# Performance work log

Measured on AMD Instinct MI355X. Metric: run time of the kernel, lower is better.

Reference implementation:

```python
import jax, jax.numpy as jnp
import numpy as np

B, S, D, H = 2, 2048, 1024, 16
HD = D // H  # 64
SOFT_CAP = 50.0
MAX_WAVELENGTH = 10000.0


def apply_rope(x, positions, head_dim):
    # x: [B,S,H,hd], positions: [B,S]
    fraction = 2.0 * jnp.arange(head_dim // 2, dtype=jnp.float32) / head_dim
    timescale = MAX_WAVELENGTH ** fraction                      # [hd/2]
    sinusoid = positions.astype(jnp.float32)[..., None] / timescale  # [B,S,hd/2]
    sin = jnp.sin(sinusoid)[..., None, :]                       # [B,S,1,hd/2]
    cos = jnp.cos(sinusoid)[..., None, :]
    first, second = jnp.split(x, 2, axis=-1)
    out = jnp.concatenate(
        [first * cos - second * sin, second * cos + first * sin], axis=-1)
    return out.astype(x.dtype)


def setup_inputs() -> dict:
    key = jax.random.key(0)
    k1, k2, k3 = jax.random.split(key, 3)
    inputs = jax.random.normal(k1, (B, S, D), jnp.float32)
    segment_positions = jnp.tile(jnp.arange(S, dtype=jnp.int32), (B, 1))
    mask = jnp.tril(jnp.ones((S, S), dtype=bool))[None, None]   # causal [1,1,S,S]
    w_in = jax.random.normal(k2, (D, H, 3 * HD), jnp.float32) * 0.02
    w_out = jax.random.normal(k3, (H, HD, D), jnp.float32) * 0.02
    return {"inputs": inputs, "segment_positions": segment_positions,
            "mask": mask, "w_in": w_in, "w_out": w_out}


def reference(inputs, segment_positions, mask, w_in, w_out):
    # fused QKV projection: [B,S,H,3*hd]
    proj = jnp.einsum('bsd,dhe->bshe', inputs, w_in)
    q, k, v = jnp.split(proj, 3, axis=-1)
    q = apply_rope(q, segment_positions, HD)
    k = apply_rope(k, segment_positions, HD)
    q = q / jnp.sqrt(jnp.float32(HD))
    attn = jnp.einsum('bqhd,bkhd->bhqk', q, k)                  # [B,H,S,S]
    big_neg = jnp.finfo(jnp.float32).min
    attn = jnp.where(mask, attn, big_neg)
    attn = jnp.tanh(attn / SOFT_CAP) * SOFT_CAP                 # soft-cap AFTER mask
    attn = jax.nn.softmax(attn, axis=-1)
    x = jnp.einsum('bhqk,bkhd->bqhd', attn, v)
    return jnp.einsum('bqhd,hdo->bqo', x, w_out)
```

## Files before the change

kernel.cpp:

```cpp
#include <hip/hip_runtime.h>
#include <math.h>

#define BB 2
#define SS 2048
#define DD 1024
#define HH 16
#define HDIM 64
#define BS (BB*SS)
#define NQKV (HH*3*HDIM)
#define PERHEAD ((size_t)SS*HDIM)

typedef __attribute__((ext_vector_type(8))) short bf16x8;
typedef __attribute__((ext_vector_type(4))) float f32x4;

typedef const __attribute__((address_space(1))) unsigned int ga_u32;
typedef __attribute__((address_space(3))) unsigned int lds_u32;

__device__ inline short f2bf(float x) {
    union { float f; unsigned u; } v; v.f = x;
    unsigned r = v.u + 0x7FFF + ((v.u >> 16) & 1);
    return (short)(r >> 16);
}

__device__ inline void gl_lds16(const void* g, void* l) {
    __builtin_amdgcn_global_load_lds((ga_u32*)g, (lds_u32*)l, 16, 0, 0);
}

__global__ __launch_bounds__(256)
void convert_bf16(const float* __restrict__ A, unsigned short* __restrict__ Ab)
{
    int i = (blockIdx.x * 256 + threadIdx.x) * 4;
    float4 v = *(const float4*)&A[i];
    ushort4 o;
    o.x = (unsigned short)f2bf(v.x); o.y = (unsigned short)f2bf(v.y);
    o.z = (unsigned short)f2bf(v.z); o.w = (unsigned short)f2bf(v.w);
    *(ushort4*)&Ab[i] = o;
}

__global__ __launch_bounds__(256)
void transpose_bf16(const float* __restrict__ W, unsigned short* __restrict__ Wt,
                    int K, int N)
{
    __shared__ float tile[64][65];
    const int k0 = blockIdx.y * 64, n0 = blockIdx.x * 64;
    const int t = threadIdx.x;
    #pragma unroll
    for (int i = 0; i < 4; ++i) {
        int lin = t + 256 * i;
        int r = lin >> 4, c4 = (lin & 15) << 2;
        float4 v = *(const float4*)&W[(size_t)(k0 + r) * N + n0 + c4];
        tile[r][c4] = v.x; tile[r][c4 + 1] = v.y;
        tile[r][c4 + 2] = v.z; tile[r][c4 + 3] = v.w;
    }
    __syncthreads();
    #pragma unroll
    for (int i = 0; i < 4; ++i) {
        int lin = t + 256 * i;
        int n = lin >> 4, c4 = (lin & 15) << 2;
        ushort4 o;
        o.x = (unsigned short)f2bf(tile[c4 + 0][n]);
        o.y = (unsigned short)f2bf(tile[c4 + 1][n]);
        o.z = (unsigned short)f2bf(tile[c4 + 2][n]);
        o.w = (unsigned short)f2bf(tile[c4 + 3][n]);
        *(ushort4*)&Wt[(size_t)(n0 + n) * K + k0 + c4] = o;
    }
}

template<int QKV>
__global__ __launch_bounds__(256)
void gemm_mfma(const unsigned short* __restrict__ A,
               const unsigned short* __restrict__ Bt,
               float* __restrict__ C,
               float* __restrict__ Qp, float* __restrict__ Kp,
               unsigned short* __restrict__ Vb,
               int M, int N, int K)
{
    __shared__ __align__(16) unsigned short As[128 * 32];
    __shared__ __align__(16) unsigned short Bs[128 * 32];
    const int t = threadIdx.x;
    const int wave = t >> 6, lane = t & 63;
    const int quad = lane >> 4, lc = lane & 15;
    const int bm = blockIdx.y * 128, bn = blockIdx.x * 128;
    const int wr = wave >> 1, wc = wave & 1;

    const int srow0 = wave * 32 + (lane >> 2);
    const int srow1 = srow0 + 16;
    const int sc = (lane & 3) ^ ((lane >> 3) & 3);
    const unsigned short* aptr0 = A  + (size_t)(bm + srow0) * K + sc * 8;
    const unsigned short* aptr1 = A  + (size_t)(bm + srow1) * K + sc * 8;
    const unsigned short* bptr0 = Bt + (size_t)(bn + srow0) * K + sc * 8;
    const unsigned short* bptr1 = Bt + (size_t)(bn + srow1) * K + sc * 8;
    unsigned short* alds0 = &As[(wave * 32)      * 32];
    unsigned short* alds1 = &As[(wave * 32 + 16) * 32];
    unsigned short* blds0 = &Bs[(wave * 32)      * 32];
    unsigned short* blds1 = &Bs[(wave * 32 + 16) * 32];

    const int cx = quad ^ ((lc >> 1) & 3);

    f32x4 acc[4][4] = {};

    for (int k0 = 0; k0 < K; k0 += 32) {
        gl_lds16(aptr0 + k0, alds0);
        gl_lds16(aptr1 + k0, alds1);
        gl_lds16(bptr0 + k0, blds0);
        gl_lds16(bptr1 + k0, blds1);
        __syncthreads();

        bf16x8 af[4], bfr[4];
        #pragma unroll
        for (int rt = 0; rt < 4; ++rt)
            af[rt] = *(const bf16x8*)&As[(wr * 64 + rt * 16 + lc) * 32 + cx * 8];
        #pragma unroll
        for (int nt = 0; nt < 4; ++nt)
            bfr[nt] = *(const bf16x8*)&Bs[(wc * 64 + nt * 16 + lc) * 32 + cx * 8];
        #pragma unroll
        for (int rt = 0; rt < 4; ++rt)
            #pragma unroll
            for (int nt = 0; nt < 4; ++nt)
                acc[rt][nt] = __builtin_amdgcn_mfma_f32_16x16x32_bf16(
                    af[rt], bfr[nt], acc[rt][nt], 0, 0, 0);
        __syncthreads();
    }

    if (QKV) {
        #pragma unroll
        for (int rt = 0; rt < 4; ++rt) {
            #pragma unroll
            for (int reg = 0; reg < 4; ++reg) {
                int m = bm + wr * 64 + rt * 16 + quad * 4 + reg;
                int b = m >> 11, s = m & 2047;
                #pragma unroll
                for (int nt = 0; nt < 4; ++nt) {
                    int n = bn + wc * 64 + nt * 16 + lc;
                    int h = n / 192, r = n % 192;
                    float v = acc[rt][nt][reg];
                    if (r < 64) {
                        Qp[(((size_t)(b * HH + h)) * SS + s) * HDIM + r] = v;
                    } else if (r < 128) {
                        Kp[(((size_t)(b * HH + h)) * SS + s) * HDIM + r - 64] = v;
                    } else {
                        Vb[(((size_t)(b * HH + h)) * HDIM + (r - 128)) * SS + s] =
                            (unsigned short)f2bf(v);
                    }
                }
            }
        }
    } else {
        #pragma unroll
        for (int rt = 0; rt < 4; ++rt)
            #pragma unroll
            for (int reg = 0; reg < 4; ++reg) {
                int m = bm + wr * 64 + rt * 16 + quad * 4 + reg;
                #pragma unroll
                for (int nt = 0; nt < 4; ++nt) {
                    int n = bn + wc * 64 + nt * 16 + lc;
                    C[(size_t)m * N + n] = acc[rt][nt][reg];
                }
            }
    }
}

__global__ __launch_bounds__(256)
void rope_kernel(const float* __restrict__ Qf, const float* __restrict__ Kf,
                 unsigned short* __restrict__ Qb, unsigned short* __restrict__ Kb,
                 const int* __restrict__ pos)
{
    int tid = blockIdx.x * 256 + threadIdx.x;
    int i = tid & 31;
    int s = (tid >> 5) & 2047;
    int h = (tid >> 16) & 15;
    int b = tid >> 20;
    float p  = (float)pos[b * SS + s];
    float ts = powf(10000.0f, (float)i / 32.0f);
    float ang = p / ts;
    float sn, cs;
    sincosf(ang, &sn, &cs);
    size_t base = (((size_t)(b * HH + h)) * SS + s) * HDIM;
    float q1 = Qf[base + i], q2 = Qf[base + 32 + i];
    Qb[base + i]      = (unsigned short)f2bf((q1 * cs - q2 * sn) * 0.125f);
    Qb[base + 32 + i] = (unsigned short)f2bf((q2 * cs + q1 * sn) * 0.125f);
    float k1 = Kf[base + i], k2 = Kf[base + 32 + i];
    Kb[base + i]      = (unsigned short)f2bf(k1 * cs - k2 * sn);
    Kb[base + 32 + i] = (unsigned short)f2bf(k2 * cs + k1 * sn);
}

__global__ __launch_bounds__(256)
void attn_mfma_kernel(const unsigned short* __restrict__ Qb,
                      const unsigned short* __restrict__ Kb,
                      const unsigned short* __restrict__ Vb,
                      unsigned short* __restrict__ Xb)
{
    __shared__ __align__(16) unsigned short Ks[64 * 64];
    __shared__ __align__(16) unsigned short Vs[64 * 64];
    __shared__ __align__(16) unsigned short Ps[4][16][72];

    const int t    = threadIdx.x;
    const int wave = t >> 6, lane = t & 63;
    const int quad = lane >> 4, lc = lane & 15;
    const int bid  = blockIdx.x;
    const int qt   = 31 - (bid >> 5);
    const int bh   = bid & 31;
    const int b    = bh >> 4, h = bh & 15;

    const unsigned short* Qbase = Qb + ((size_t)bh * SS + (size_t)(qt * 64 + wave * 16)) * HDIM;
    const unsigned short* Kbase = Kb + (size_t)bh * PERHEAD;
    const unsigned short* Vbase = Vb + (size_t)bh * PERHEAD;

    bf16x8 qf[2];
    qf[0] = *(const bf16x8*)&Qbase[lc * HDIM + quad * 8];
    qf[1] = *(const bf16x8*)&Qbase[lc * HDIM + 32 + quad * 8];

    const int r8 = lane >> 3, c8 = lane & 7, gcs = c8 ^ r8;
    const unsigned short* ksrc0 = Kbase + (size_t)(wave * 16 + r8) * HDIM + gcs * 8;
    const unsigned short* ksrc1 = ksrc0 + 8 * HDIM;
    unsigned short* kdst0 = &Ks[(wave * 16) * 64];
    unsigned short* kdst1 = &Ks[(wave * 16 + 8) * 64];
    const unsigned short* vsrc0 = Vbase + (size_t)(wave * 16 + r8) * SS + gcs * 8;
    const unsigned short* vsrc1 = vsrc0 + 8 * SS;
    unsigned short* vdst0 = &Vs[(wave * 16) * 64];
    unsigned short* vdst1 = &Vs[(wave * 16 + 8) * 64];

    f32x4 O[4] = {{0,0,0,0},{0,0,0,0},{0,0,0,0},{0,0,0,0}};
    float l_lane[4] = {0.f, 0.f, 0.f, 0.f};

    const int ntiles = qt + 1;
    for (int kt = 0; kt < ntiles; ++kt) {
        gl_lds16(ksrc0 + (size_t)kt * 64 * HDIM, kdst0);
        gl_lds16(ksrc1 + (size_t)kt * 64 * HDIM, kdst1);
        gl_lds16(vsrc0 + kt * 64, vdst0);
        gl_lds16(vsrc1 + kt * 64, vdst1);
        __syncthreads();

        f32x4 S[4];
        #pragma unroll
        for (int kg = 0; kg < 4; ++kg) {
            S[kg] = (f32x4){0.f, 0.f, 0.f, 0.f};
            #pragma unroll
            for (int khd = 0; khd < 2; ++khd) {
                int pc = ((khd << 2) | quad) ^ (lc & 7);
                bf16x8 kf = *(const bf16x8*)&Ks[(kg * 16 + lc) * 64 + pc * 8];
                S[kg] = __builtin_amdgcn_mfma_f32_16x16x32_bf16(qf[khd], kf, S[kg], 0, 0, 0);
            }
        }

        const bool diag = (kt == qt);
        #pragma unroll
        for (int kg = 0; kg < 4; ++kg) {
            #pragma unroll
            for (int r = 0; r < 4; ++r) {
                float s  = S[kg][r];
                float e  = __builtin_amdgcn_exp2f(s * 0.057707801f);
                float rc = __builtin_amdgcn_rcpf(e + 1.0f);
                float p  = __builtin_amdgcn_exp2f(fmaf(-144.2695041f, rc, 72.13475205f));
                if (diag && (kg * 16 + lc > wave * 16 + quad * 4 + r)) p = 0.f;
                l_lane[r] += p;
                Ps[wave][quad * 4 + r][kg * 16 + lc] = (unsigned short)f2bf(p);
            }
        }

        bf16x8 pf0 = *(const bf16x8*)&Ps[wave][lc][quad * 8];
        bf16x8 pf1 = *(const bf16x8*)&Ps[wave][lc][32 + quad * 8];
        #pragma unroll
        for (int g = 0; g < 4; ++g) {
            int p0 = quad ^ (lc & 7);
            int p1 = (4 | quad) ^ (lc & 7);
            bf16x8 vf0 = *(const bf16x8*)&Vs[(g * 16 + lc) * 64 + p0 * 8];
            bf16x8 vf1 = *(const bf16x8*)&Vs[(g * 16 + lc) * 64 + p1 * 8];
            O[g] = __builtin_amdgcn_mfma_f32_16x16x32_bf16(pf0, vf0, O[g], 0, 0, 0);
            O[g] = __builtin_amdgcn_mfma_f32_16x16x32_bf16(pf1, vf1, O[g], 0, 0, 0);
        }
        __syncthreads();
    }

    #pragma unroll
    for (int r = 0; r < 4; ++r) {
        float l = l_lane[r];
        l += __shfl_xor(l, 1); l += __shfl_xor(l, 2);
        l += __shfl_xor(l, 4); l += __shfl_xor(l, 8);
        float inv = __builtin_amdgcn_rcpf(l);
        int q_g = qt * 64 + wave * 16 + quad * 4 + r;
        size_t base = ((size_t)b * SS + q_g) * DD + h * HDIM;
        #pragma unroll
        for (int g = 0; g < 4; ++g)
            Xb[base + g * 16 + lc] = (unsigned short)f2bf(O[g][r] * inv);
    }
}

extern "C" void kernel_launch(void* const* d_in, const int* in_sizes, int n_in,
                              void* d_out, int out_size, void* d_ws, size_t ws_size,
                              hipStream_t stream)
{
    const float* inputs = (const float*)d_in[0];
    const int*   pos    = (const int*)d_in[1];
    const float* w_in   = (const float*)d_in[3];
    const float* w_out  = (const float*)d_in[4];
    float* out = (float*)d_out;

    const size_t NELT = (size_t)BB * HH * SS * HDIM;
    float* base = (float*)d_ws;
    float* Qf = base;
    float* Kf = base + NELT;
    unsigned short* Vb    = (unsigned short*)(base + 2 * NELT);
    unsigned short* Ab    = (unsigned short*)(base + 2 * NELT + NELT / 2);
    unsigned short* Wt_in = Ab + NELT;
    unsigned short* Qb    = Ab;
    unsigned short* Kb    = Ab + NELT;
    unsigned short* Wt_out= (unsigned short*)(base + 2 * NELT + NELT / 2 + NELT);
    unsigned short* Xb    = (unsigned short*)Qf;

    dim3 blk(256);
    convert_bf16<<<dim3((BS * DD) / 1024), blk, 0, stream>>>(inputs, Ab);
    transpose_bf16<<<dim3(NQKV / 64, DD / 64), blk, 0, stream>>>(w_in, Wt_in, DD, NQKV);
    transpose_bf16<<<dim3(DD / 64, DD / 64), blk, 0, stream>>>(w_out, Wt_out, DD, DD);
    gemm_mfma<1><<<dim3(NQKV / 128, BS / 128), blk, 0, stream>>>(
        Ab, Wt_in, nullptr, Qf, Kf, Vb, BS, NQKV, DD);
    rope_kernel<<<dim3((BB * HH * SS * 32) / 256), blk, 0, stream>>>(
        Qf, Kf, Qb, Kb, pos);
    attn_mfma_kernel<<<dim3(SS / 64 * BB * HH), blk, 0, stream>>>(Qb, Kb, Vb, Xb);
    gemm_mfma<0><<<dim3(DD / 128, BS / 128), blk, 0, stream>>>(
        Xb, Wt_out, out, nullptr, nullptr, nullptr, BS, DD, DD);
}
```

Before: 231.8 us.

## Fuse RoPE into QKV GEMM epilogue and restructure attention with paired tiles

```diff
diff --git a/kernel.cpp b/kernel.cpp
--- a/kernel.cpp
+++ b/kernel.cpp
@@ -11,6 +11,7 @@
 #define PERHEAD ((size_t)SS*HDIM)
 
 typedef __attribute__((ext_vector_type(8))) short bf16x8;
+typedef __attribute__((ext_vector_type(4))) short bf16x4;
 typedef __attribute__((ext_vector_type(4))) float f32x4;
 
 typedef const __attribute__((address_space(1))) unsigned int ga_u32;
@@ -24,6 +25,29 @@
 
 __device__ inline void gl_lds16(const void* g, void* l) {
     __builtin_amdgcn_global_load_lds((ga_u32*)g, (lds_u32*)l, 16, 0, 0);
+}
+
+__device__ inline f32x4 mfma16(bf16x4 a, bf16x4 b, f32x4 c) {
+#if __has_builtin(__builtin_amdgcn_mfma_f32_16x16x16bf16_1k)
+    return __builtin_amdgcn_mfma_f32_16x16x16bf16_1k(a, b, c, 0, 0, 0);
+#else
+    f32x4 d;
+    asm("v_mfma_f32_16x16x16_bf16 %0, %1, %2, %3"
+        : "=v"(d) : "v"(a), "v"(b), "v"(c));
+    return d;
+#endif
+}
+
+__global__ __launch_bounds__(256)
+void sincos_table(const int* __restrict__ pos, float2* __restrict__ tab)
+{
+    int idx = blockIdx.x * 256 + threadIdx.x;
+    int i = idx & 31, s = (idx >> 5) & 2047, b = idx >> 16;
+    float p  = (float)pos[b * SS + s];
+    float ts = powf(10000.0f, (float)i / 32.0f);
+    float sn, cs;
+    sincosf(p / ts, &sn, &cs);
+    tab[idx] = make_float2(cs, sn);
 }
 
 __global__ __launch_bounds__(256)
@@ -71,8 +95,9 @@
 void gemm_mfma(const unsigned short* __restrict__ A,
                const unsigned short* __restrict__ Bt,
                float* __restrict__ C,
-               float* __restrict__ Qp, float* __restrict__ Kp,
+               unsigned short* __restrict__ Qb, unsigned short* __restrict__ Kb,
                unsigned short* __restrict__ Vb,
+               const float2* __restrict__ tab,
                int M, int N, int K)
 {
     __shared__ __align__(16) unsigned short As[128 * 32];
@@ -123,24 +148,35 @@
     }
 
     if (QKV) {
+        const int cb = blockIdx.x * 2 + wc;
+        const int h = cb / 3, part = cb % 3;
         #pragma unroll
         for (int rt = 0; rt < 4; ++rt) {
             #pragma unroll
             for (int reg = 0; reg < 4; ++reg) {
                 int m = bm + wr * 64 + rt * 16 + quad * 4 + reg;
                 int b = m >> 11, s = m & 2047;
-                #pragma unroll
-                for (int nt = 0; nt < 4; ++nt) {
-                    int n = bn + wc * 64 + nt * 16 + lc;
-                    int h = n / 192, r = n % 192;
-                    float v = acc[rt][nt][reg];
-                    if (r < 64) {
-                        Qp[(((size_t)(b * HH + h)) * SS + s) * HDIM + r] = v;
-                    } else if (r < 128) {
-                        Kp[(((size_t)(b * HH + h)) * SS + s) * HDIM + r - 64] = v;
-                    } else {
-                        Vb[(((size_t)(b * HH + h)) * HDIM + (r - 128)) * SS + s] =
-                            (unsigned short)f2bf(v);
+                if (part == 2) {
+                    #pragma unroll
+                    for (int nt = 0; nt < 4; ++nt) {
+                        int r = nt * 16 + lc;
+                        Vb[(((size_t)(b * HH + h)) * HDIM + r) * SS + s] =
+                            (unsigned short)f2bf(acc[rt][nt][reg]);
+                    }
+                } else {
+                    unsigned short* dst = part == 0 ? Qb : Kb;
+                    const float scale = part == 0 ? 0.125f : 1.0f;
+                    size_t rowbase = (((size_t)(b * HH + h)) * SS + s) * HDIM;
+                    #pragma unroll
+                    for (int nt = 0; nt < 2; ++nt) {
+                        int i = nt * 16 + lc;
+                        float2 cssn = tab[((size_t)(b * SS + s)) * 32 + i];
+                        float first  = acc[rt][nt][reg];
+                        float second = acc[rt][nt + 2][reg];
+                        dst[rowbase + i] =
+                            (unsigned short)f2bf((first * cssn.x - second * cssn.y) * scale);
+                        dst[rowbase + i + 32] =
+                            (unsigned short)f2bf((second * cssn.x + first * cssn.y) * scale);
                     }
                 }
             }
@@ -161,128 +197,118 @@
 }
 
 __global__ __launch_bounds__(256)
-void rope_kernel(const float* __restrict__ Qf, const float* __restrict__ Kf,
-                 unsigned short* __restrict__ Qb, unsigned short* __restrict__ Kb,
-                 const int* __restrict__ pos)
-{
-    int tid = blockIdx.x * 256 + threadIdx.x;
-    int i = tid & 31;
-    int s = (tid >> 5) & 2047;
-    int h = (tid >> 16) & 15;
-    int b = tid >> 20;
-    float p  = (float)pos[b * SS + s];
-    float ts = powf(10000.0f, (float)i / 32.0f);
-    float ang = p / ts;
-    float sn, cs;
-    sincosf(ang, &sn, &cs);
-    size_t base = (((size_t)(b * HH + h)) * SS + s) * HDIM;
-    float q1 = Qf[base + i], q2 = Qf[base + 32 + i];
-    Qb[base + i]      = (unsigned short)f2bf((q1 * cs - q2 * sn) * 0.125f);
-    Qb[base + 32 + i] = (unsigned short)f2bf((q2 * cs + q1 * sn) * 0.125f);
-    float k1 = Kf[base + i], k2 = Kf[base + 32 + i];
-    Kb[base + i]      = (unsigned short)f2bf(k1 * cs - k2 * sn);
-    Kb[base + 32 + i] = (unsigned short)f2bf(k2 * cs + k1 * sn);
-}
-
-__global__ __launch_bounds__(256)
 void attn_mfma_kernel(const unsigned short* __restrict__ Qb,
                       const unsigned short* __restrict__ Kb,
                       const unsigned short* __restrict__ Vb,
                       unsigned short* __restrict__ Xb)
 {
-    __shared__ __align__(16) unsigned short Ks[64 * 64];
-    __shared__ __align__(16) unsigned short Vs[64 * 64];
-    __shared__ __align__(16) unsigned short Ps[4][16][72];
+    __shared__ __align__(16) unsigned short Ks[2][64 * 64];
+    __shared__ __align__(16) unsigned short Vs[2][64 * 64];
 
     const int t    = threadIdx.x;
     const int wave = t >> 6, lane = t & 63;
     const int quad = lane >> 4, lc = lane & 15;
-    const int bid  = blockIdx.x;
-    const int qt   = 31 - (bid >> 5);
-    const int bh   = bid & 31;
+    const int pair = blockIdx.x >> 5;
+    const int bh   = blockIdx.x & 31;
     const int b    = bh >> 4, h = bh & 15;
 
-    const unsigned short* Qbase = Qb + ((size_t)bh * SS + (size_t)(qt * 64 + wave * 16)) * HDIM;
     const unsigned short* Kbase = Kb + (size_t)bh * PERHEAD;
     const unsigned short* Vbase = Vb + (size_t)bh * PERHEAD;
 
-    bf16x8 qf[2];
-    qf[0] = *(const bf16x8*)&Qbase[lc * HDIM + quad * 8];
-    qf[1] = *(const bf16x8*)&Qbase[lc * HDIM + 32 + quad * 8];
-
     const int r8 = lane >> 3, c8 = lane & 7, gcs = c8 ^ r8;
-    const unsigned short* ksrc0 = Kbase + (size_t)(wave * 16 + r8) * HDIM + gcs * 8;
-    const unsigned short* ksrc1 = ksrc0 + 8 * HDIM;
-    unsigned short* kdst0 = &Ks[(wave * 16) * 64];
-    unsigned short* kdst1 = &Ks[(wave * 16 + 8) * 64];
-    const unsigned short* vsrc0 = Vbase + (size_t)(wave * 16 + r8) * SS + gcs * 8;
-    const unsigned short* vsrc1 = vsrc0 + 8 * SS;
-    unsigned short* vdst0 = &Vs[(wave * 16) * 64];
-    unsigned short* vdst1 = &Vs[(wave * 16 + 8) * 64];
-
-    f32x4 O[4] = {{0,0,0,0},{0,0,0,0},{0,0,0,0},{0,0,0,0}};
-    float l_lane[4] = {0.f, 0.f, 0.f, 0.f};
-
-    const int ntiles = qt + 1;
-    for (int kt = 0; kt < ntiles; ++kt) {
-        gl_lds16(ksrc0 + (size_t)kt * 64 * HDIM, kdst0);
-        gl_lds16(ksrc1 + (size_t)kt * 64 * HDIM, kdst1);
-        gl_lds16(vsrc0 + kt * 64, vdst0);
-        gl_lds16(vsrc1 + kt * 64, vdst1);
+
+    #pragma unroll
+    for (int phase = 0; phase < 2; ++phase) {
+        const int qt = phase ? pair : (31 - pair);
+
+        const unsigned short* Qbase =
+            Qb + ((size_t)bh * SS + (size_t)(qt * 64 + wave * 16)) * HDIM;
+        bf16x8 qf[2];
+        qf[0] = *(const bf16x8*)&Qbase[lc * HDIM + quad * 8];
+        qf[1] = *(const bf16x8*)&Qbase[lc * HDIM + 32 + quad * 8];
+
+        f32x4 O[4] = {{0,0,0,0},{0,0,0,0},{0,0,0,0},{0,0,0,0}};
+        float l = 0.0f;
+
         __syncthreads();
-
-        f32x4 S[4];
-        #pragma unroll
-        for (int kg = 0; kg < 4; ++kg) {
-            S[kg] = (f32x4){0.f, 0.f, 0.f, 0.f};
-            #pragma unroll
-            for (int khd = 0; khd < 2; ++khd) {
-                int pc = ((khd << 2) | quad) ^ (lc & 7);
-                bf16x8 kf = *(const bf16x8*)&Ks[(kg * 16 + lc) * 64 + pc * 8];
-                S[kg] = __builtin_amdgcn_mfma_f32_16x16x32_bf16(qf[khd], kf, S[kg], 0, 0, 0);
-            }
+        {
+            const unsigned short* ks = Kbase + (size_t)(wave * 16 + r8) * HDIM + gcs * 8;
+            gl_lds16(ks,            &Ks[0][(wave * 16)     * 64]);
+            gl_lds16(ks + 8 * HDIM, &Ks[0][(wave * 16 + 8) * 64]);
+            const unsigned short* vs = Vbase + (size_t)(wave * 16 + r8) * SS + gcs * 8;
+            gl_lds16(vs,          &Vs[0][(wave * 16)     * 64]);
+            gl_lds16(vs + 8 * SS, &Vs[0][(wave * 16 + 8) * 64]);
         }
 
-        const bool diag = (kt == qt);
-        #pragma unroll
-        for (int kg = 0; kg < 4; ++kg) {
-            #pragma unroll
-            for (int r = 0; r < 4; ++r) {
-                float s  = S[kg][r];
-                float e  = __builtin_amdgcn_exp2f(s * 0.057707801f);
-                float rc = __builtin_amdgcn_rcpf(e + 1.0f);
-                float p  = __builtin_amdgcn_exp2f(fmaf(-144.2695041f, rc, 72.13475205f));
-                if (diag && (kg * 16 + lc > wave * 16 + quad * 4 + r)) p = 0.f;
-                l_lane[r] += p;
-                Ps[wave][quad * 4 + r][kg * 16 + lc] = (unsigned short)f2bf(p);
+        for (int kt = 0; kt <= qt; ++kt) {
+            __syncthreads();
+            const int buf = kt & 1;
+            if (kt < qt) {
+                const int nb = buf ^ 1;
+                const unsigned short* ks =
+                    Kbase + (size_t)((kt + 1) * 64 + wave * 16 + r8) * HDIM + gcs * 8;
+                gl_lds16(ks,            &Ks[nb][(wave * 16)     * 64]);
+                gl_lds16(ks + 8 * HDIM, &Ks[nb][(wave * 16 + 8) * 64]);
+                const unsigned short* vs =
+                    Vbase + (size_t)(wave * 16 + r8) * SS + (kt + 1) * 64 + gcs * 8;
+                gl_lds16(vs,          &Vs[nb][(wave * 16)     * 64]);
+                gl_lds16(vs + 8 * SS, &Vs[nb][(wave * 16 + 8) * 64]);
+            }
+
+            f32x4 St[4];
+            #pragma unroll
+            for (int kg = 0; kg < 4; ++kg) {
+                St[kg] = (f32x4){0.f, 0.f, 0.f, 0.f};
+                #pragma unroll
+                for (int khd = 0; khd < 2; ++khd) {
+                    int pc = ((khd << 2) | quad) ^ (lc & 7);
+                    bf16x8 kf = *(const bf16x8*)&Ks[buf][(kg * 16 + lc) * 64 + pc * 8];
+                    St[kg] = __builtin_amdgcn_mfma_f32_16x16x32_bf16(
+                        kf, qf[khd], St[kg], 0, 0, 0);
+                }
+            }
+
+            const bool diag = (kt == qt);
+            bf16x4 pf[4];
+            #pragma unroll
+            for (int kg = 0; kg < 4; ++kg) {
+                #pragma unroll
+                for (int reg = 0; reg < 4; ++reg) {
+                    float s  = St[kg][reg];
+                    float e  = __builtin_amdgcn_exp2f(s * 0.057707801f);
+                    float rc = __builtin_amdgcn_rcpf(e + 1.0f);
+                    float p  = __builtin_amdgcn_exp2f(
+                                   fmaf(-144.2695041f, rc, 72.13475205f));
+                    if (diag && (kg * 16 + quad * 4 + reg > wave * 16 + lc)) p = 0.f;
+                    l += p;
+                    pf[kg][reg] = f2bf(p);
+                }
+            }
+
+            #pragma unroll
+            for (int g = 0; g < 4; ++g) {
+                #pragma unroll
+                for (int kg = 0; kg < 4; ++kg) {
+                    int pc2 = (kg * 2 + (quad >> 1)) ^ (lc & 7);
+                    bf16x4 vf = *(const bf16x4*)
+                        &Vs[buf][(g * 16 + lc) * 64 + pc2 * 8 + (quad & 1) * 4];
+                    O[g] = mfma16(pf[kg], vf, O[g]);
+                }
             }
         }
 
-        bf16x8 pf0 = *(const bf16x8*)&Ps[wave][lc][quad * 8];
-        bf16x8 pf1 = *(const bf16x8*)&Ps[wave][lc][32 + quad * 8];
-        #pragma unroll
-        for (int g = 0; g < 4; ++g) {
-            int p0 = quad ^ (lc & 7);
-            int p1 = (4 | quad) ^ (lc & 7);
-            bf16x8 vf0 = *(const bf16x8*)&Vs[(g * 16 + lc) * 64 + p0 * 8];
-            bf16x8 vf1 = *(const bf16x8*)&Vs[(g * 16 + lc) * 64 + p1 * 8];
-            O[g] = __builtin_amdgcn_mfma_f32_16x16x32_bf16(pf0, vf0, O[g], 0, 0, 0);
-            O[g] = __builtin_amdgcn_mfma_f32_16x16x32_bf16(pf1, vf1, O[g], 0, 0, 0);
+        l += __shfl_xor(l, 16);
+        l += __shfl_xor(l, 32);
+        #pragma unroll
+        for (int reg = 0; reg < 4; ++reg) {
+            float lq  = __shfl(l, quad * 4 + reg);
+            float inv = __builtin_amdgcn_rcpf(lq);
+            int q_g = qt * 64 + wave * 16 + quad * 4 + reg;
+            size_t base = ((size_t)b * SS + q_g) * DD + h * HDIM;
+            #pragma unroll
+            for (int g = 0; g < 4; ++g)
+                Xb[base + g * 16 + lc] = (unsigned short)f2bf(O[g][reg] * inv);
         }
-        __syncthreads();
-    }
-
-    #pragma unroll
-    for (int r = 0; r < 4; ++r) {
-        float l = l_lane[r];
-        l += __shfl_xor(l, 1); l += __shfl_xor(l, 2);
-        l += __shfl_xor(l, 4); l += __shfl_xor(l, 8);
-        float inv = __builtin_amdgcn_rcpf(l);
-        int q_g = qt * 64 + wave * 16 + quad * 4 + r;
-        size_t base = ((size_t)b * SS + q_g) * DD + h * HDIM;
-        #pragma unroll
-        for (int g = 0; g < 4; ++g)
-            Xb[base + g * 16 + lc] = (unsigned short)f2bf(O[g][r] * inv);
     }
 }
 
@@ -297,26 +323,23 @@
     float* out = (float*)d_out;
 
     const size_t NELT = (size_t)BB * HH * SS * HDIM;
-    float* base = (float*)d_ws;
-    float* Qf = base;
-    float* Kf = base + NELT;
-    unsigned short* Vb    = (unsigned short*)(base + 2 * NELT);
-    unsigned short* Ab    = (unsigned short*)(base + 2 * NELT + NELT / 2);
-    unsigned short* Wt_in = Ab + NELT;
-    unsigned short* Qb    = Ab;
-    unsigned short* Kb    = Ab + NELT;
-    unsigned short* Wt_out= (unsigned short*)(base + 2 * NELT + NELT / 2 + NELT);
-    unsigned short* Xb    = (unsigned short*)Qf;
+    unsigned short* Ab     = (unsigned short*)d_ws;
+    unsigned short* Wt_in  = Ab + NELT;
+    unsigned short* Wt_out = Wt_in + (size_t)NQKV * DD;
+    unsigned short* Qb     = Wt_out + (size_t)DD * DD;
+    unsigned short* Kb     = Qb + NELT;
+    unsigned short* Vb     = Kb + NELT;
+    unsigned short* Xb     = Vb + NELT;
+    float2*         tab    = (float2*)(Xb + NELT);
 
     dim3 blk(256);
+    sincos_table<<<dim3((BB * SS * 32) / 256), blk, 0, stream>>>(pos, tab);
     convert_bf16<<<dim3((BS * DD) / 1024), blk, 0, stream>>>(inputs, Ab);
     transpose_bf16<<<dim3(NQKV / 64, DD / 64), blk, 0, stream>>>(w_in, Wt_in, DD, NQKV);
     transpose_bf16<<<dim3(DD / 64, DD / 64), blk, 0, stream>>>(w_out, Wt_out, DD, DD);
     gemm_mfma<1><<<dim3(NQKV / 128, BS / 128), blk, 0, stream>>>(
-        Ab, Wt_in, nullptr, Qf, Kf, Vb, BS, NQKV, DD);
-    rope_kernel<<<dim3((BB * HH * SS * 32) / 256), blk, 0, stream>>>(
-        Qf, Kf, Qb, Kb, pos);
-    attn_mfma_kernel<<<dim3(SS / 64 * BB * HH), blk, 0, stream>>>(Qb, Kb, Vb, Xb);
+        Ab, Wt_in, nullptr, Qb, Kb, Vb, tab, BS, NQKV, DD);
+    attn_mfma_kernel<<<dim3(16 * BB * HH), blk, 0, stream>>>(Qb, Kb, Vb, Xb);
     gemm_mfma<0><<<dim3(DD / 128, BS / 128), blk, 0, stream>>>(
-        Xb, Wt_out, out, nullptr, nullptr, nullptr, BS, DD, DD);
-}
+        Xb, Wt_out, out, nullptr, nullptr, nullptr, nullptr, BS, DD, DD);
+}
```

New measurement: 229.4 us. About the same (-1.0%).
